# Performance work log

Measured on AMD Instinct MI355X. Metric: run time of the kernel, lower is better.

The kernel has to match this reference:

```python
import jax, jax.numpy as jnp
import numpy as np


def setup_inputs() -> dict:
    key = jax.random.key(0)
    ks = jax.random.split(key, 8)
    B, L, F, H, A = 128, 196, 2048, 512, 512
    features = jax.random.normal(ks[0], (B, L, F), dtype=jnp.float32)
    hidden_state = jax.random.normal(ks[1], (B, H), dtype=jnp.float32)
    # Linear params (PyTorch layout: weight [out, in], bias [out]); scaled like kaiming-uniform
    W_enc = jax.random.normal(ks[2], (A, F), dtype=jnp.float32) / np.sqrt(F)
    b_enc = jnp.zeros((A,), dtype=jnp.float32)
    W_dec = jax.random.normal(ks[3], (A, H), dtype=jnp.float32) / np.sqrt(H)
    b_dec = jnp.zeros((A,), dtype=jnp.float32)
    W_com = jax.random.normal(ks[4], (1, A), dtype=jnp.float32) / np.sqrt(A)
    b_com = jnp.zeros((1,), dtype=jnp.float32)
    return {
        "features": features, "hidden_state": hidden_state,
        "W_enc": W_enc, "b_enc": b_enc,
        "W_dec": W_dec, "b_dec": b_dec,
        "W_com": W_com, "b_com": b_com,
    }


def reference(features, hidden_state, W_enc, b_enc, W_dec, b_dec, W_com, b_com):
    # encoder_context: [B, L, A]
    enc = jnp.einsum('blf,af->bla', features, W_enc) + b_enc
    # decoder_context: [B, 1, A]
    dec = (hidden_state @ W_dec.T + b_dec)[:, None, :]
    # relu + linear to scalar score (dropout in eval mode = identity): [B, L]
    scores = jnp.einsum('bla,a->bl', jax.nn.relu(enc + dec), W_com[0]) + b_com[0]
    alpha = jax.nn.softmax(scores, axis=1)  # [B, L]
    weighted_features = jnp.einsum('blf,bl->bf', features, alpha)  # [B, F]
    return weighted_features, alpha
```

## Files before the change

kernel.cpp:

```cpp
#include <hip/hip_runtime.h>
#include <hip/hip_bf16.h>
#include <math.h>

#define B_  128
#define L_  196
#define F_  2048
#define H_  512
#define A_  512
#define ML_ (B_*L_)

typedef _Float16 half8 __attribute__((ext_vector_type(8)));
typedef _Float16 half4v __attribute__((ext_vector_type(4)));
typedef _Float16 half2v __attribute__((ext_vector_type(2)));
typedef float f32x4 __attribute__((ext_vector_type(4)));

__device__ __forceinline__ void gld_lds16(const void* g, void* l) {
  __builtin_amdgcn_global_load_lds((const __attribute__((address_space(1))) void*)g,
                                   (__attribute__((address_space(3))) void*)l, 16, 0, 0);
}

__global__ __launch_bounds__(256) void k_prep(const float4* __restrict__ Wenc4,
                                              half4v* __restrict__ wH,
                                              const float* __restrict__ hs,
                                              const float* __restrict__ Wdec,
                                              const float* __restrict__ bdec,
                                              const float* __restrict__ benc,
                                              float* __restrict__ dec,
                                              float* __restrict__ scores) {
  const int b = blockIdx.x, t = threadIdx.x;

  {
    const int base = b * 2048 + t;
    float4 v[8];
#pragma unroll
    for (int j = 0; j < 8; j++) v[j] = Wenc4[base + j * 256];
#pragma unroll
    for (int j = 0; j < 8; j++) {
      half4v o = { (_Float16)v[j].x, (_Float16)v[j].y, (_Float16)v[j].z, (_Float16)v[j].w };
      wH[base + j * 256] = o;
    }
  }

  const int g = b * 256 + t;
  if (g < ML_) scores[g] = 0.f;

  __shared__ float h[H_];
  h[t]       = hs[b * H_ + t];
  h[t + 256] = hs[b * H_ + t + 256];
  __syncthreads();

#pragma unroll
  for (int r = 0; r < 2; r++) {
    const int a = t + r * 256;
    float acc = bdec[a] + benc[a];
    const float4* wr = (const float4*)(Wdec + (size_t)a * H_);
#pragma unroll 4
    for (int k4 = 0; k4 < H_ / 4; k4++) {
      const float4 w = wr[k4];
      acc += w.x * h[4*k4] + w.y * h[4*k4+1] + w.z * h[4*k4+2] + w.w * h[4*k4+3];
    }
    dec[b * A_ + a] = acc;
  }
}

__global__ __launch_bounds__(256) void k_scores_mfma(const float* __restrict__ fA,
                                                     const _Float16* __restrict__ fB,
                                                     const float* __restrict__ dec,
                                                     const float* __restrict__ wcom,
                                                     float* __restrict__ scores) {
  __shared__ _Float16  As[128 * 64];
  __shared__ _Float16  Bs[128 * 64];
  __shared__ float decS[2][128];

  const int tid  = threadIdx.x;
  const int lane = tid & 63;
  const int w    = tid >> 6;

  const int l = blockIdx.x;
  int at_, mt;
  if (l < 768) { at_ = (l >> 3) & 3; mt = (l >> 5) * 8 + (l & 7); }
  else { const int idx = l - 768; at_ = idx >> 2; mt = 192 + (idx & 3); }
  const int a0 = at_ * 128;
  const int m0 = mt * 128;

  const int wm   = w & 1;
  const int wn   = w >> 1;
  const int quad = lane >> 4;
  const int l16  = lane & 15;

  f32x4 acc[4][4];
#pragma unroll
  for (int i = 0; i < 4; i++)
#pragma unroll
    for (int j = 0; j < 4; j++)
#pragma unroll
      for (int k = 0; k < 4; k++) acc[i][j][k] = 0.f;

  const int b0 = m0 / L_;
  {
    const int i = tid >> 7;
    const int j = tid & 127;
    int bb = b0 + i; if (bb > B_ - 1) bb = B_ - 1;
    decS[i][j] = dec[bb * A_ + a0 + j];
  }

  const int arow = tid >> 1;
  const int ah   = tid & 1;
  const int ar7  = arow & 7;
  const float* aP = fA + (size_t)(m0 + arow) * F_ + ah * 32;
  const int srowB = lane >> 3;
  const _Float16* pB = fB + (size_t)(a0 + w * 32 + srowB) * F_
                          + (size_t)(((lane & 7) ^ srowB) * 8);

  float4 fr[8];
#pragma unroll
  for (int jj = 0; jj < 8; jj++) fr[jj] = *(const float4*)(aP + jj * 4);

  for (int kt = 0; kt < F_; kt += 64) {
#pragma unroll
    for (int i = 0; i < 4; i++)
      gld_lds16(pB + (size_t)(i * 8) * F_ + kt, &Bs[(w * 32 + i * 8) * 64]);

#pragma unroll
    for (int j = 0; j < 4; j++) {
      union { half8 v; half2v h2[4]; } u;
      u.h2[0] = (half2v)__builtin_amdgcn_cvt_pkrtz(fr[2*j].x,   fr[2*j].y);
      u.h2[1] = (half2v)__builtin_amdgcn_cvt_pkrtz(fr[2*j].z,   fr[2*j].w);
      u.h2[2] = (half2v)__builtin_amdgcn_cvt_pkrtz(fr[2*j+1].x, fr[2*j+1].y);
      u.h2[3] = (half2v)__builtin_amdgcn_cvt_pkrtz(fr[2*j+1].z, fr[2*j+1].w);
      *(half8*)&As[arow * 64 + (((ah << 2) | j) ^ ar7) * 8] = u.v;
    }
    __syncthreads();

    if (kt + 64 < F_) {
#pragma unroll
      for (int jj = 0; jj < 8; jj++)
        fr[jj] = *(const float4*)(aP + kt + 64 + jj * 4);
    }

#pragma unroll
    for (int kk = 0; kk < 2; kk++) {
      half8 af[4], bf[4];
#pragma unroll
      for (int mf = 0; mf < 4; mf++) {
        const int row = wm * 64 + mf * 16 + l16;
        af[mf] = *(const half8*)&As[row * 64 + ((((kk << 2) | quad)) ^ (row & 7)) * 8];
      }
#pragma unroll
      for (int at = 0; at < 4; at++) {
        const int row = wn * 64 + at * 16 + l16;
        bf[at] = *(const half8*)&Bs[row * 64 + ((((kk << 2) | quad)) ^ (row & 7)) * 8];
      }
#pragma unroll
      for (int mf = 0; mf < 4; mf++)
#pragma unroll
        for (int at = 0; at < 4; at++)
          acc[mf][at] = __builtin_amdgcn_mfma_f32_16x16x32_f16(af[mf], bf[at], acc[mf][at], 0, 0, 0);
    }
    __syncthreads();
  }

  float w4[4];
#pragma unroll
  for (int at = 0; at < 4; at++) w4[at] = wcom[a0 + wn * 64 + at * 16 + l16];

#pragma unroll
  for (int mf = 0; mf < 4; mf++) {
#pragma unroll
    for (int r = 0; r < 4; r++) {
      const int m  = m0 + wm * 64 + mf * 16 + quad * 4 + r;
      const int db = m / L_ - b0;
      float p = 0.f;
#pragma unroll
      for (int at = 0; at < 4; at++) {
        const float e = acc[mf][at][r] + decS[db][wn * 64 + at * 16 + l16];
        p = fmaf(fmaxf(e, 0.f), w4[at], p);
      }
      p += __shfl_xor(p, 1);
      p += __shfl_xor(p, 2);
      p += __shfl_xor(p, 4);
      p += __shfl_xor(p, 8);
      if (l16 == 0) atomicAdd(&scores[m], p);
    }
  }
}

__global__ __launch_bounds__(256) void k_softmax(const float* __restrict__ scores,
                                                 float* __restrict__ alpha) {
  const int b = blockIdx.x, t = threadIdx.x;
  __shared__ float redm[4];
  __shared__ float reds[4];

  float s = (t < L_) ? scores[b * L_ + t] : -INFINITY;
  float m = s;
#pragma unroll
  for (int o = 32; o >= 1; o >>= 1) m = fmaxf(m, __shfl_xor(m, o));
  if ((t & 63) == 0) redm[t >> 6] = m;
  __syncthreads();
  m = fmaxf(fmaxf(redm[0], redm[1]), fmaxf(redm[2], redm[3]));
  float e = (t < L_) ? expf(s - m) : 0.f;
  float sum = e;
#pragma unroll
  for (int o = 32; o >= 1; o >>= 1) sum += __shfl_xor(sum, o);
  if ((t & 63) == 0) reds[t >> 6] = sum;
  __syncthreads();
  sum = reds[0] + reds[1] + reds[2] + reds[3];
  if (t < L_) alpha[b * L_ + t] = e / sum;
}

__global__ __launch_bounds__(128) void k_attn_f32(const float* __restrict__ feat,
                                                  const float* __restrict__ alpha,
                                                  float* __restrict__ out) {
  const int fc = blockIdx.x, b = blockIdx.y, t = threadIdx.x;
  __shared__ float al[L_];

  al[t] = alpha[b * L_ + t];
  if (t < L_ - 128) al[t + 128] = alpha[b * L_ + t + 128];
  __syncthreads();

  const int f0 = fc * 256 + t * 2;
  const float2* fp = (const float2*)(feat + (size_t)b * L_ * F_ + f0);
  float a0x = 0.f, a0y = 0.f, a1x = 0.f, a1y = 0.f;
#pragma unroll 7
  for (int ll = 0; ll < 98; ll++) {
    const float2 v0 = fp[(size_t)ll * (F_ / 2)];
    const float2 v1 = fp[(size_t)(ll + 98) * (F_ / 2)];
    const float w0 = al[ll];
    const float w1 = al[ll + 98];
    a0x = fmaf(v0.x, w0, a0x);
    a0y = fmaf(v0.y, w0, a0y);
    a1x = fmaf(v1.x, w1, a1x);
    a1y = fmaf(v1.y, w1, a1y);
  }
  float2 o = { a0x + a1x, a0y + a1y };
  *(float2*)(out + (size_t)b * F_ + f0) = o;
}

__global__ __launch_bounds__(256) void k_scores_f32(const float* __restrict__ feat,
                                                    const float* __restrict__ Wenc,
                                                    const float* __restrict__ dec,
                                                    const float* __restrict__ wcom,
                                                    float* __restrict__ scores) {
  __shared__ float As[16][128];
  __shared__ float Bs[16][128];
  const int tid = threadIdx.x;
  const int m0 = blockIdx.x * 128;
  const int a0 = blockIdx.y * 128;
  const int tx = tid & 15;
  const int ty = tid >> 4;
  float acc[8][8];
#pragma unroll
  for (int i = 0; i < 8; i++)
#pragma unroll
    for (int j = 0; j < 8; j++) acc[i][j] = 0.f;
  for (int kt = 0; kt < F_; kt += 16) {
#pragma unroll
    for (int rep = 0; rep < 2; rep++) {
      const int idx = rep * 256 + tid;
      const int row = idx >> 2;
      const int kp  = (idx & 3) << 2;
      const float4 v = *(const float4*)(feat + (size_t)(m0 + row) * F_ + kt + kp);
      As[kp+0][row] = v.x; As[kp+1][row] = v.y; As[kp+2][row] = v.z; As[kp+3][row] = v.w;
      const float4 w = *(const float4*)(Wenc + (size_t)(a0 + row) * F_ + kt + kp);
      Bs[kp+0][row] = w.x; Bs[kp+1][row] = w.y; Bs[kp+2][row] = w.z; Bs[kp+3][row] = w.w;
    }
    __syncthreads();
#pragma unroll
    for (int k = 0; k < 16; k++) {
      float ar[8], br[8];
      *(float4*)&ar[0] = *(const float4*)&As[k][ty * 8];
      *(float4*)&ar[4] = *(const float4*)&As[k][ty * 8 + 4];
      *(float4*)&br[0] = *(const float4*)&Bs[k][tx * 8];
      *(float4*)&br[4] = *(const float4*)&Bs[k][tx * 8 + 4];
#pragma unroll
      for (int i = 0; i < 8; i++)
#pragma unroll
        for (int j = 0; j < 8; j++) acc[i][j] = fmaf(ar[i], br[j], acc[i][j]);
    }
    __syncthreads();
  }
  float w8[8];
  *(float4*)&w8[0] = *(const float4*)(wcom + a0 + tx * 8);
  *(float4*)&w8[4] = *(const float4*)(wcom + a0 + tx * 8 + 4);
#pragma unroll
  for (int i = 0; i < 8; i++) {
    const int m = m0 + ty * 8 + i;
    const int b = m / L_;
    const float* dp = dec + b * A_ + a0 + tx * 8;
    float p = 0.f;
#pragma unroll
    for (int j = 0; j < 8; j++) {
      const float e = acc[i][j] + dp[j];
      p = fmaf(fmaxf(e, 0.f), w8[j], p);
    }
    p += __shfl_xor(p, 1);
    p += __shfl_xor(p, 2);
    p += __shfl_xor(p, 4);
    p += __shfl_xor(p, 8);
    if (tx == 0) atomicAdd(&scores[m], p);
  }
}

__global__ __launch_bounds__(256) void k_dec_only(const float* __restrict__ hs,
                                                  const float* __restrict__ Wdec,
                                                  const float* __restrict__ bdec,
                                                  const float* __restrict__ benc,
                                                  float* __restrict__ dec,
                                                  float* __restrict__ scores) {
  const int b = blockIdx.x, t = threadIdx.x;
  const int g = b * 256 + t;
  if (g < ML_) scores[g] = 0.f;
  __shared__ float h[H_];
  h[t]       = hs[b * H_ + t];
  h[t + 256] = hs[b * H_ + t + 256];
  __syncthreads();
#pragma unroll
  for (int r = 0; r < 2; r++) {
    const int a = t + r * 256;
    float acc = bdec[a] + benc[a];
    const float4* wr = (const float4*)(Wdec + (size_t)a * H_);
#pragma unroll 4
    for (int k4 = 0; k4 < H_ / 4; k4++) {
      const float4 w = wr[k4];
      acc += w.x * h[4*k4] + w.y * h[4*k4+1] + w.z * h[4*k4+2] + w.w * h[4*k4+3];
    }
    dec[b * A_ + a] = acc;
  }
}

extern "C" void kernel_launch(void* const* d_in, const int* in_sizes, int n_in,
                              void* d_out, int out_size, void* d_ws, size_t ws_size,
                              hipStream_t stream) {
  const float* feat = (const float*)d_in[0];
  const float* hs   = (const float*)d_in[1];
  const float* Wenc = (const float*)d_in[2];
  const float* benc = (const float*)d_in[3];
  const float* Wdec = (const float*)d_in[4];
  const float* bdec = (const float*)d_in[5];
  const float* wcom = (const float*)d_in[6];

  float* out   = (float*)d_out;
  float* alpha = out + B_ * F_;
  float* dec    = (float*)d_ws;
  float* scores = dec + B_ * A_;

  const size_t need = (size_t)(B_ * A_ + ML_) * 4 + (size_t)A_ * F_ * 2;

  if (ws_size >= need) {
    _Float16* wH = (_Float16*)(scores + ML_);
    k_prep<<<dim3(128), dim3(256), 0, stream>>>(
        (const float4*)Wenc, (half4v*)wH, hs, Wdec, bdec, benc, dec, scores);
    k_scores_mfma<<<dim3(784), dim3(256), 0, stream>>>(feat, wH, dec, wcom, scores);
  } else {
    k_dec_only<<<dim3(B_), dim3(256), 0, stream>>>(hs, Wdec, bdec, benc, dec, scores);
    k_scores_f32<<<dim3(ML_ / 128, A_ / 128), dim3(256), 0, stream>>>(feat, Wenc, dec, wcom, scores);
  }
  k_softmax<<<dim3(B_), dim3(256), 0, stream>>>(scores, alpha);
  k_attn_f32<<<dim3(8, B_), dim3(128), 0, stream>>>(feat, alpha, out);
}
```

Baseline: 472.1 us.

## Double-buffer fp32 A and fp16 B tiles via direct global-to-LDS loads

The scores GEMM kernel now streams the fp32 feature tile straight into LDS with global_load_lds instead of staging it in registers, converting to fp16 when fragments are read from LDS. Both A and B tiles are double-buffered with a K-step of 32. A vmcnt wait lets the next step's loads overlap the current MFMAs, and there is one barrier pair per step. This frees the VGPRs that held the register prefetch and aims to hide global latency, at the cost of twice the fp32 LDS footprint, fp16 conversion repeated for every fragment read, and one redundant clamped load at the final step.

```diff
diff --git a/kernel.cpp b/kernel.cpp
--- a/kernel.cpp
+++ b/kernel.cpp
@@ -68,8 +68,8 @@
                                                      const float* __restrict__ dec,
                                                      const float* __restrict__ wcom,
                                                      float* __restrict__ scores) {
-  __shared__ _Float16  As[128 * 64];
-  __shared__ _Float16  Bs[128 * 64];
+  __shared__ float     As[2][128 * 32];
+  __shared__ _Float16  Bs[2][128 * 32];
   __shared__ float decS[2][128];
 
   const int tid  = threadIdx.x;
@@ -104,60 +104,67 @@
     decS[i][j] = dec[bb * A_ + a0 + j];
   }
 
-  const int arow = tid >> 1;
-  const int ah   = tid & 1;
-  const int ar7  = arow & 7;
-  const float* aP = fA + (size_t)(m0 + arow) * F_ + ah * 32;
-  const int srowB = lane >> 3;
+  const int srowA = lane >> 3;
+  const float* pA = fA + (size_t)(m0 + w * 32 + srowA) * F_
+                       + (size_t)(((lane & 7) ^ srowA) * 4);
+  const int srowB = lane >> 2;
   const _Float16* pB = fB + (size_t)(a0 + w * 32 + srowB) * F_
-                          + (size_t)(((lane & 7) ^ srowB) * 8);
-
-  float4 fr[8];
-#pragma unroll
-  for (int jj = 0; jj < 8; jj++) fr[jj] = *(const float4*)(aP + jj * 4);
-
-  for (int kt = 0; kt < F_; kt += 64) {
+                          + (size_t)(((lane & 3) ^ (srowB & 3)) * 8);
+
+#pragma unroll
+  for (int i = 0; i < 4; i++)
+    gld_lds16(pA + (size_t)(i * 8) * F_, &As[0][(w * 32 + i * 8) * 32]);
+#pragma unroll
+  for (int i = 0; i < 2; i++)
+    gld_lds16(pB + (size_t)(i * 16) * F_, &Bs[0][(w * 32 + i * 16) * 32]);
+
+  auto kstep = [&](int buf, int spre) {
 #pragma unroll
     for (int i = 0; i < 4; i++)
-      gld_lds16(pB + (size_t)(i * 8) * F_ + kt, &Bs[(w * 32 + i * 8) * 64]);
-
-#pragma unroll
-    for (int j = 0; j < 4; j++) {
+      gld_lds16(pA + (size_t)(i * 8) * F_ + spre * 32,
+                &As[buf ^ 1][(w * 32 + i * 8) * 32]);
+#pragma unroll
+    for (int i = 0; i < 2; i++)
+      gld_lds16(pB + (size_t)(i * 16) * F_ + spre * 32,
+                &Bs[buf ^ 1][(w * 32 + i * 16) * 32]);
+    asm volatile("s_waitcnt vmcnt(6)" ::: "memory");
+    __builtin_amdgcn_s_barrier();
+    __builtin_amdgcn_sched_barrier(0);
+
+    half8 af[4], bf[4];
+#pragma unroll
+    for (int mf = 0; mf < 4; mf++) {
+      const int row = wm * 64 + mf * 16 + l16;
+      const int s0  = (quad * 2) ^ (row & 7);
+      const float4 f0 = *(const float4*)&As[buf][row * 32 + s0 * 4];
+      const float4 f1 = *(const float4*)&As[buf][row * 32 + (s0 ^ 1) * 4];
       union { half8 v; half2v h2[4]; } u;
-      u.h2[0] = (half2v)__builtin_amdgcn_cvt_pkrtz(fr[2*j].x,   fr[2*j].y);
-      u.h2[1] = (half2v)__builtin_amdgcn_cvt_pkrtz(fr[2*j].z,   fr[2*j].w);
-      u.h2[2] = (half2v)__builtin_amdgcn_cvt_pkrtz(fr[2*j+1].x, fr[2*j+1].y);
-      u.h2[3] = (half2v)__builtin_amdgcn_cvt_pkrtz(fr[2*j+1].z, fr[2*j+1].w);
-      *(half8*)&As[arow * 64 + (((ah << 2) | j) ^ ar7) * 8] = u.v;
-    }
-    __syncthreads();
-
-    if (kt + 64 < F_) {
-#pragma unroll
-      for (int jj = 0; jj < 8; jj++)
-        fr[jj] = *(const float4*)(aP + kt + 64 + jj * 4);
-    }
-
-#pragma unroll
-    for (int kk = 0; kk < 2; kk++) {
-      half8 af[4], bf[4];
-#pragma unroll
-      for (int mf = 0; mf < 4; mf++) {
-        const int row = wm * 64 + mf * 16 + l16;
-        af[mf] = *(const half8*)&As[row * 64 + ((((kk << 2) | quad)) ^ (row & 7)) * 8];
-      }
-#pragma unroll
-      for (int at = 0; at < 4; at++) {
-        const int row = wn * 64 + at * 16 + l16;
-        bf[at] = *(const half8*)&Bs[row * 64 + ((((kk << 2) | quad)) ^ (row & 7)) * 8];
-      }
-#pragma unroll
-      for (int mf = 0; mf < 4; mf++)
-#pragma unroll
-        for (int at = 0; at < 4; at++)
-          acc[mf][at] = __builtin_amdgcn_mfma_f32_16x16x32_f16(af[mf], bf[at], acc[mf][at], 0, 0, 0);
-    }
-    __syncthreads();
+      u.h2[0] = (half2v)__builtin_amdgcn_cvt_pkrtz(f0.x, f0.y);
+      u.h2[1] = (half2v)__builtin_amdgcn_cvt_pkrtz(f0.z, f0.w);
+      u.h2[2] = (half2v)__builtin_amdgcn_cvt_pkrtz(f1.x, f1.y);
+      u.h2[3] = (half2v)__builtin_amdgcn_cvt_pkrtz(f1.z, f1.w);
+      af[mf] = u.v;
+    }
+#pragma unroll
+    for (int at = 0; at < 4; at++) {
+      const int row = wn * 64 + at * 16 + l16;
+      const int sb  = quad ^ (row & 3);
+      bf[at] = *(const half8*)&Bs[buf][row * 32 + sb * 8];
+    }
+#pragma unroll
+    for (int mf = 0; mf < 4; mf++)
+#pragma unroll
+      for (int at = 0; at < 4; at++)
+        acc[mf][at] = __builtin_amdgcn_mfma_f32_16x16x32_f16(af[mf], bf[at], acc[mf][at], 0, 0, 0);
+
+    __builtin_amdgcn_sched_barrier(0);
+    __builtin_amdgcn_s_barrier();
+    __builtin_amdgcn_sched_barrier(0);
+  };
+
+  for (int s = 0; s < 64; s += 2) {
+    kstep(0, s + 1);
+    kstep(1, s + 2 < 64 ? s + 2 : 63);
   }
 
   float w4[4];
```

Result: no change. 467.0 us (-1.1%).

## Double-buffer B tile and prefetch next K-step with explicit waitcnt

Applied to the files above, without the earlier changes.

Double-buffers the LDS tile for the fp16 weight operand so the asynchronous global-to-LDS load for the next K-step is issued before the current step's MFMAs. Partial waits (vmcnt(12)) replace full __syncthreads so those loads stay in flight during compute. The fp32 feature-to-LDS staging is remapped so each wave loads 4-float chunks from 32 rows with a new swizzle, which changes coalescing and LDS store patterns. This costs another 16KB of LDS per block, and the hand-counted vmcnt is fragile if the compiler reorders or changes the number of loads.

```diff
diff --git a/kernel.cpp b/kernel.cpp
--- a/kernel.cpp
+++ b/kernel.cpp
@@ -69,7 +69,7 @@
                                                      const float* __restrict__ wcom,
                                                      float* __restrict__ scores) {
   __shared__ _Float16  As[128 * 64];
-  __shared__ _Float16  Bs[128 * 64];
+  __shared__ _Float16  Bs[2][128 * 64];
   __shared__ float decS[2][128];
 
   const int tid  = threadIdx.x;
@@ -104,39 +104,47 @@
     decS[i][j] = dec[bb * A_ + a0 + j];
   }
 
-  const int arow = tid >> 1;
-  const int ah   = tid & 1;
-  const int ar7  = arow & 7;
-  const float* aP = fA + (size_t)(m0 + arow) * F_ + ah * 32;
+  const int arow4 = lane >> 4;
+  const int acol  = (lane & 15) * 4;
+  const float* pA = fA + (size_t)(m0 + w * 32 + arow4) * F_ + acol;
+  const int g8    = lane & 15;
+
   const int srowB = lane >> 3;
   const _Float16* pB = fB + (size_t)(a0 + w * 32 + srowB) * F_
                           + (size_t)(((lane & 7) ^ srowB) * 8);
 
   float4 fr[8];
 #pragma unroll
-  for (int jj = 0; jj < 8; jj++) fr[jj] = *(const float4*)(aP + jj * 4);
-
-  for (int kt = 0; kt < F_; kt += 64) {
-#pragma unroll
-    for (int i = 0; i < 4; i++)
-      gld_lds16(pB + (size_t)(i * 8) * F_ + kt, &Bs[(w * 32 + i * 8) * 64]);
-
-#pragma unroll
-    for (int j = 0; j < 4; j++) {
-      union { half8 v; half2v h2[4]; } u;
-      u.h2[0] = (half2v)__builtin_amdgcn_cvt_pkrtz(fr[2*j].x,   fr[2*j].y);
-      u.h2[1] = (half2v)__builtin_amdgcn_cvt_pkrtz(fr[2*j].z,   fr[2*j].w);
-      u.h2[2] = (half2v)__builtin_amdgcn_cvt_pkrtz(fr[2*j+1].x, fr[2*j+1].y);
-      u.h2[3] = (half2v)__builtin_amdgcn_cvt_pkrtz(fr[2*j+1].z, fr[2*j+1].w);
-      *(half8*)&As[arow * 64 + (((ah << 2) | j) ^ ar7) * 8] = u.v;
-    }
-    __syncthreads();
-
-    if (kt + 64 < F_) {
-#pragma unroll
-      for (int jj = 0; jj < 8; jj++)
-        fr[jj] = *(const float4*)(aP + kt + 64 + jj * 4);
-    }
+  for (int i = 0; i < 8; i++)
+    fr[i] = *(const float4*)(pA + (size_t)(i * 4) * F_);
+#pragma unroll
+  for (int i = 0; i < 4; i++)
+    gld_lds16(pB + (size_t)(i * 8) * F_, &Bs[0][(w * 32 + i * 8) * 64]);
+
+  auto kstep = [&](int kt, int buf, bool last) {
+#pragma unroll
+    for (int i = 0; i < 8; i++) {
+      const int r = w * 32 + i * 4 + arow4;
+      half4v h;
+      half2v h0 = (half2v)__builtin_amdgcn_cvt_pkrtz(fr[i].x, fr[i].y);
+      half2v h1 = (half2v)__builtin_amdgcn_cvt_pkrtz(fr[i].z, fr[i].w);
+      h[0] = h0[0]; h[1] = h0[1]; h[2] = h1[0]; h[3] = h1[1];
+      *(half4v*)&As[r * 64 + (g8 ^ ((r & 7) << 1)) * 4] = h;
+    }
+    if (!last) {
+#pragma unroll
+      for (int i = 0; i < 8; i++)
+        fr[i] = *(const float4*)(pA + (size_t)(i * 4) * F_ + kt + 64);
+#pragma unroll
+      for (int i = 0; i < 4; i++)
+        gld_lds16(pB + (size_t)(i * 8) * F_ + kt + 64,
+                  &Bs[buf ^ 1][(w * 32 + i * 8) * 64]);
+      asm volatile("s_waitcnt vmcnt(12) lgkmcnt(0)" ::: "memory");
+    } else {
+      asm volatile("s_waitcnt vmcnt(0) lgkmcnt(0)" ::: "memory");
+    }
+    __builtin_amdgcn_s_barrier();
+    __builtin_amdgcn_sched_barrier(0);
 
 #pragma unroll
     for (int kk = 0; kk < 2; kk++) {
@@ -144,12 +152,12 @@
 #pragma unroll
       for (int mf = 0; mf < 4; mf++) {
         const int row = wm * 64 + mf * 16 + l16;
-        af[mf] = *(const half8*)&As[row * 64 + ((((kk << 2) | quad)) ^ (row & 7)) * 8];
+        af[mf] = *(const half8*)&As[row * 64 + (((kk * 4 + quad)) ^ (row & 7)) * 8];
       }
 #pragma unroll
       for (int at = 0; at < 4; at++) {
         const int row = wn * 64 + at * 16 + l16;
-        bf[at] = *(const half8*)&Bs[row * 64 + ((((kk << 2) | quad)) ^ (row & 7)) * 8];
+        bf[at] = *(const half8*)&Bs[buf][row * 64 + (((kk * 4 + quad)) ^ (row & 7)) * 8];
       }
 #pragma unroll
       for (int mf = 0; mf < 4; mf++)
@@ -157,8 +165,15 @@
         for (int at = 0; at < 4; at++)
           acc[mf][at] = __builtin_amdgcn_mfma_f32_16x16x32_f16(af[mf], bf[at], acc[mf][at], 0, 0, 0);
     }
-    __syncthreads();
-  }
+
+    __builtin_amdgcn_sched_barrier(0);
+    __builtin_amdgcn_s_barrier();
+    __builtin_amdgcn_sched_barrier(0);
+  };
+
+  int kt = 0;
+  for (int s = 0; s < 31; ++s, kt += 64) kstep(kt, s & 1, false);
+  kstep(kt, 31 & 1, true);
 
   float w4[4];
 #pragma unroll
```

After: 428.1 us. 1.1x faster.
